# Performance work log

Hardware: AMD Instinct MI355X
Metric: run time of the kernel (lower is better)

## Reference

```python
import jax, jax.numpy as jnp
import numpy as np

N_NODES = 100000
FEAT_DIM = 3
HID = 128
S1 = 50  # enc1 neighbor samples
S2 = 10  # enc2 neighbor samples


def setup_inputs() -> dict:
    key = jax.random.key(0)
    ks = jax.random.split(key, 12)
    inp = {
        "nodes": jnp.arange(N_NODES, dtype=jnp.int64) if jax.config.jax_enable_x64 else jnp.arange(N_NODES, dtype=jnp.int32),
        "features": jax.random.normal(ks[0], (N_NODES, FEAT_DIM), dtype=jnp.float32),
        "neigh1": jax.random.randint(ks[1], (N_NODES, S1), 0, N_NODES),
        "neigh2": jax.random.randint(ks[2], (N_NODES, S2), 0, N_NODES),
        "W1": jax.random.normal(ks[3], (HID, FEAT_DIM), dtype=jnp.float32) * 0.5,
        "W2": jax.random.normal(ks[4], (HID, HID), dtype=jnp.float32) * 0.08,
        "w_a": jax.random.normal(ks[5], (128, HID + 1), dtype=jnp.float32) * 0.08,
        "b_a": jax.random.normal(ks[6], (128,), dtype=jnp.float32) * 0.01,
        "w_b": jax.random.normal(ks[7], (64, 128), dtype=jnp.float32) * 0.08,
        "b_b": jax.random.normal(ks[8], (64,), dtype=jnp.float32) * 0.01,
        "w_c": jax.random.normal(ks[9], (1, 64), dtype=jnp.float32) * 0.1,
        "b_c": jax.random.normal(ks[10], (1,), dtype=jnp.float32) * 0.01,
        "partition_size": 500,
        "n_partition_edges": 137,
    }
    return inp


def reference(nodes, features, neigh1, neigh2, W1, W2, w_a, b_a, w_b, b_b, w_c, b_c,
              partition_size, n_partition_edges):
    # ---- enc1 (GraphSAGE mean, gcn=True: self node included in mean) over all nodes
    nf1 = features[neigh1]                       # [N, S1, F] irregular gather
    agg1 = (nf1.sum(axis=1) + features) / (neigh1.shape[1] + 1)  # [N, F]
    h1 = jax.nn.relu(agg1 @ W1.T)                # [N, HID]

    # ---- enc2 over the query nodes
    nf2 = h1[neigh2[nodes]]                      # [n, S2, HID] irregular gather
    agg2 = (nf2.sum(axis=1) + h1[nodes]) / (neigh2.shape[1] + 1)  # [n, HID]
    emb = jax.nn.relu(agg2 @ W2.T)               # [n, HID]

    # ---- append remaining-space column, MLP, softmax over all nodes (dim 0)
    remaining_space = jnp.asarray(partition_size - n_partition_edges, dtype=emb.dtype)
    col = jnp.full((emb.shape[0], 1), remaining_space, dtype=emb.dtype)
    x = jnp.concatenate([emb, col], axis=1)      # [n, HID+1]
    x = jax.nn.relu(x @ w_a.T + b_a)
    x = jax.nn.relu(x @ w_b.T + b_b)
    scores = (x @ w_c.T + b_c)[:, 0]             # [n]
    return jax.nn.softmax(scores, axis=0)
```

## Files before the change

### kernel.cpp

```cpp
#include <hip/hip_runtime.h>
#include <math.h>

#define N_NODES 100000
#define S1 50
#define S2 10
#define HID 128
#define NT 64
#define AST 66

#define W2_ELEMS   (128 * 128)
#define WA_ELEMS   (129 * 128)
#define WB_ELEMS   (128 * 64)
#define PAD_ELEMS  (W2_ELEMS + WA_ELEMS + WB_ELEMS)

__device__ __forceinline__ unsigned long long dkey(double d) {
    unsigned long long u = __double_as_longlong(d);
    return (u & 0x8000000000000000ULL) ? ~u : (u | 0x8000000000000000ULL);
}
__device__ __forceinline__ double dunkey(unsigned long long k) {
    return (k & 0x8000000000000000ULL)
        ? __longlong_as_double(k & 0x7FFFFFFFFFFFFFFFULL)
        : __longlong_as_double(~k);
}

__global__ __launch_bounds__(256) void pack_kernel(
    const float* __restrict__ feat,
    const float* __restrict__ W2, const float* __restrict__ w_a,
    const float* __restrict__ w_b,
    double* __restrict__ wt, float4* __restrict__ feat4,
    unsigned long long* __restrict__ gmaxu, double* __restrict__ gsum)
{
    int i = blockIdx.x * 256 + threadIdx.x;
    if (i == 0) { gmaxu[0] = 0ULL; gsum[0] = 0.0; }
    if (i < W2_ELEMS) {
        int k = i >> 7, o = i & 127;
        wt[i] = (double)W2[o * 128 + k];
    } else if (i < W2_ELEMS + WA_ELEMS) {
        int j = i - W2_ELEMS;
        int k = j >> 7, o = j & 127;
        wt[i] = (double)w_a[o * 129 + k];
    } else if (i < PAD_ELEMS) {
        int j = i - W2_ELEMS - WA_ELEMS;
        int k = j >> 6, o = j & 63;
        wt[i] = (double)w_b[o * 128 + k];
    } else if (i < PAD_ELEMS + N_NODES) {
        int n = i - PAD_ELEMS;
        float4 v = { feat[n * 3 + 0], feat[n * 3 + 1], feat[n * 3 + 2], 0.0f };
        feat4[n] = v;
    }
}

__global__ __launch_bounds__(64) void gather_kernel(
    const float4* __restrict__ feat4, const int* __restrict__ neigh1,
    double* __restrict__ agg1d)
{
    const int n = blockIdx.x * 64 + threadIdx.x;
    if (n >= N_NODES) return;
    const int* __restrict__ row = &neigh1[n * S1];
    double f0, f1, f2;
    { float4 v = feat4[n]; f0 = (double)v.x; f1 = (double)v.y; f2 = (double)v.z; }
    #pragma unroll 10
    for (int j = 0; j < S1; j++) {
        float4 v = feat4[row[j]];
        f0 += (double)v.x; f1 += (double)v.y; f2 += (double)v.z;
    }
    const double r51 = 1.0 / 51.0;
    agg1d[n * 3 + 0] = f0 * r51;
    agg1d[n * 3 + 1] = f1 * r51;
    agg1d[n * 3 + 2] = f2 * r51;
}

__global__ __launch_bounds__(256, 1) void enc2_mlp_kernel(
    const int* __restrict__ nodes, const int* __restrict__ neigh2,
    const double* __restrict__ agg1d,
    const float* __restrict__ W1, const double* __restrict__ wt,
    const float* __restrict__ b_a, const float* __restrict__ b_b,
    const float* __restrict__ w_c, const float* __restrict__ b_c,
    const int* __restrict__ psz, const int* __restrict__ npe,
    double* __restrict__ scoresd, unsigned long long* __restrict__ gmaxu)
{
    __shared__ __align__(16) double sX[HID * AST];
    __shared__ double sS[4];
    double* sG = sX;

    const double* __restrict__ Wt2 = wt;
    const double* __restrict__ Wta = wt + W2_ELEMS;
    const double* __restrict__ Wtb = wt + W2_ELEMS + WA_ELEMS;

    const int tid  = threadIdx.x;
    const int base = blockIdx.x * NT;

    for (int t = tid; t < NT * (S2 + 1); t += 256) {
        int ns = t / 11, j = t - ns * 11;
        int gi = base + ns;
        int node = nodes[gi < N_NODES ? gi : N_NODES - 1];
        int src  = (j == 0) ? node : neigh2[node * S2 + (j - 1)];
        sG[t * 4 + 0] = agg1d[src * 3 + 0];
        sG[t * 4 + 1] = agg1d[src * 3 + 1];
        sG[t * 4 + 2] = agg1d[src * 3 + 2];
    }
    __syncthreads();

    {
        const int n = tid & 63;
        double g0[11], g1[11], g2[11];
        #pragma unroll
        for (int j = 0; j < 11; j++) {
            g0[j] = sG[(n * 11 + j) * 4 + 0];
            g1[j] = sG[(n * 11 + j) * 4 + 1];
            g2[j] = sG[(n * 11 + j) * 4 + 2];
        }
        __syncthreads();
        const int part = tid >> 6;
        #pragma unroll
        for (int s = 0; s < 32; s++) {
            int t = part * 32 + s;
            double wx = (double)W1[t * 3 + 0];
            double wy = (double)W1[t * 3 + 1];
            double wz = (double)W1[t * 3 + 2];
            double acc = 0.0;
            #pragma unroll
            for (int j = 0; j < 11; j++)
                acc += fmax(wx * g0[j] + wy * g1[j] + wz * g2[j], 0.0);
            sX[t * AST + n] = acc / 11.0;
        }
    }
    __syncthreads();

    const int og = tid & 31;
    const int ng = tid >> 5;
    const int n0 = 8 * ng;
    const int o0 = 2 * og;

    {
        double acc[4][8] = {};
        const double* __restrict__ wk = &Wt2[o0];
        const double* __restrict__ ak = &sX[n0];
        double2 wc0 = *(const double2*)&wk[0];
        double2 wc1 = *(const double2*)&wk[64];
        double2 wd0 = *(const double2*)&wk[128];
        double2 wd1 = *(const double2*)&wk[128 + 64];
        double2 ac[4];
        #pragma unroll
        for (int i = 0; i < 4; i++) ac[i] = *(const double2*)&ak[2 * i];
        #pragma unroll 4
        for (int k = 0; k < 128; k++) {
            const int k1 = (k + 1) & 127;
            const int k2 = (k + 2) & 127;
            double2 wn0 = *(const double2*)&wk[k2 * 128];
            double2 wn1 = *(const double2*)&wk[k2 * 128 + 64];
            double2 an[4];
            #pragma unroll
            for (int i = 0; i < 4; i++)
                an[i] = *(const double2*)&ak[k1 * AST + 2 * i];
            #pragma unroll
            for (int i = 0; i < 4; i++) {
                acc[0][2*i]   += wc0.x * ac[i].x; acc[0][2*i+1] += wc0.x * ac[i].y;
                acc[1][2*i]   += wc0.y * ac[i].x; acc[1][2*i+1] += wc0.y * ac[i].y;
                acc[2][2*i]   += wc1.x * ac[i].x; acc[2][2*i+1] += wc1.x * ac[i].y;
                acc[3][2*i]   += wc1.y * ac[i].x; acc[3][2*i+1] += wc1.y * ac[i].y;
            }
            wc0 = wd0; wc1 = wd1; wd0 = wn0; wd1 = wn1;
            #pragma unroll
            for (int i = 0; i < 4; i++) ac[i] = an[i];
        }
        __syncthreads();
        #pragma unroll
        for (int i = 0; i < 4; i++) {
            int o = (i < 2) ? (o0 + i) : (64 + o0 + i - 2);
            #pragma unroll
            for (int j = 0; j < 4; j++) {
                double2 v = { fmax(acc[i][2*j], 0.0), fmax(acc[i][2*j+1], 0.0) };
                *(double2*)&sX[o * AST + n0 + 2 * j] = v;
            }
        }
    }
    __syncthreads();

    {
        double acc[4][8] = {};
        const double* __restrict__ wk = &Wta[o0];
        const double* __restrict__ ak = &sX[n0];
        double2 wc0 = *(const double2*)&wk[0];
        double2 wc1 = *(const double2*)&wk[64];
        double2 wd0 = *(const double2*)&wk[128];
        double2 wd1 = *(const double2*)&wk[128 + 64];
        double2 ac[4];
        #pragma unroll
        for (int i = 0; i < 4; i++) ac[i] = *(const double2*)&ak[2 * i];
        #pragma unroll 4
        for (int k = 0; k < 128; k++) {
            const int k1 = (k + 1) & 127;
            const int k2 = (k + 2) & 127;
            double2 wn0 = *(const double2*)&wk[k2 * 128];
            double2 wn1 = *(const double2*)&wk[k2 * 128 + 64];
            double2 an[4];
            #pragma unroll
            for (int i = 0; i < 4; i++)
                an[i] = *(const double2*)&ak[k1 * AST + 2 * i];
            #pragma unroll
            for (int i = 0; i < 4; i++) {
                acc[0][2*i]   += wc0.x * ac[i].x; acc[0][2*i+1] += wc0.x * ac[i].y;
                acc[1][2*i]   += wc0.y * ac[i].x; acc[1][2*i+1] += wc0.y * ac[i].y;
                acc[2][2*i]   += wc1.x * ac[i].x; acc[2][2*i+1] += wc1.x * ac[i].y;
                acc[3][2*i]   += wc1.y * ac[i].x; acc[3][2*i+1] += wc1.y * ac[i].y;
            }
            wc0 = wd0; wc1 = wd1; wd0 = wn0; wd1 = wn1;
            #pragma unroll
            for (int i = 0; i < 4; i++) ac[i] = an[i];
        }
        const double rem = (double)(psz[0] - npe[0]);
        double2 rl = *(const double2*)&Wta[128 * 128 + o0];
        double2 rh = *(const double2*)&Wta[128 * 128 + 64 + o0];
        const double ad[4] = {
            rl.x * rem + (double)b_a[o0],
            rl.y * rem + (double)b_a[o0 + 1],
            rh.x * rem + (double)b_a[64 + o0],
            rh.y * rem + (double)b_a[64 + o0 + 1] };
        __syncthreads();
        #pragma unroll
        for (int i = 0; i < 4; i++) {
            int o = (i < 2) ? (o0 + i) : (64 + o0 + i - 2);
            #pragma unroll
            for (int j = 0; j < 4; j++) {
                double2 v = { fmax(acc[i][2*j] + ad[i], 0.0),
                              fmax(acc[i][2*j+1] + ad[i], 0.0) };
                *(double2*)&sX[o * AST + n0 + 2 * j] = v;
            }
        }
    }
    __syncthreads();

    {
        double acc[2][8] = {};
        const double* __restrict__ wk = &Wtb[o0];
        const double* __restrict__ ak = &sX[n0];
        double2 wc = *(const double2*)&wk[0];
        double2 wd = *(const double2*)&wk[64];
        double2 ac[4];
        #pragma unroll
        for (int i = 0; i < 4; i++) ac[i] = *(const double2*)&ak[2 * i];
        #pragma unroll 4
        for (int k = 0; k < 128; k++) {
            const int k1 = (k + 1) & 127;
            const int k2 = (k + 2) & 127;
            double2 wn = *(const double2*)&wk[k2 * 64];
            double2 an[4];
            #pragma unroll
            for (int i = 0; i < 4; i++)
                an[i] = *(const double2*)&ak[k1 * AST + 2 * i];
            #pragma unroll
            for (int i = 0; i < 4; i++) {
                acc[0][2*i]   += wc.x * ac[i].x; acc[0][2*i+1] += wc.x * ac[i].y;
                acc[1][2*i]   += wc.y * ac[i].x; acc[1][2*i+1] += wc.y * ac[i].y;
            }
            wc = wd; wd = wn;
            #pragma unroll
            for (int i = 0; i < 4; i++) ac[i] = an[i];
        }
        __syncthreads();
        #pragma unroll
        for (int i = 0; i < 2; i++) {
            int o = o0 + i;
            double bb = (double)b_b[o];
            #pragma unroll
            for (int j = 0; j < 4; j++) {
                double2 v = { fmax(acc[i][2*j] + bb, 0.0),
                              fmax(acc[i][2*j+1] + bb, 0.0) };
                *(double2*)&sX[o * AST + n0 + 2 * j] = v;
            }
        }
    }
    __syncthreads();

    {
        const int j4 = tid & 3, ns = tid >> 2;
        double v = 0.0;
        #pragma unroll
        for (int r = 0; r < 16; r++)
            v += (double)w_c[j4 + 4 * r] * sX[(j4 + 4 * r) * AST + ns];
        v += __shfl_down(v, 2);
        v += __shfl_down(v, 1);
        double sc = v + (double)b_c[0];
        const bool valid = (base + ns) < N_NODES;
        if (j4 == 0 && valid)
            scoresd[base + ns] = sc;
        double vh = (j4 == 0 && valid) ? sc : -HUGE_VAL;
        #pragma unroll
        for (int off = 32; off > 0; off >>= 1)
            vh = fmax(vh, __shfl_down(vh, off));
        if ((tid & 63) == 0) sS[tid >> 6] = vh;
        __syncthreads();
        if (tid == 0)
            atomicMax(gmaxu, dkey(fmax(fmax(sS[0], sS[1]),
                                       fmax(sS[2], sS[3]))));
    }
}

__global__ __launch_bounds__(256) void exp_sum_kernel(
    double* __restrict__ s, const unsigned long long* __restrict__ gmaxu,
    double* __restrict__ gsum)
{
    __shared__ double red[4];
    const int tid = threadIdx.x;
    const double m = dunkey(gmaxu[0]);

    double acc = 0.0;
    for (int i = blockIdx.x * 256 + tid; i < N_NODES; i += gridDim.x * 256) {
        double e = exp(s[i] - m);
        s[i] = e;
        acc += e;
    }
    #pragma unroll
    for (int off = 32; off > 0; off >>= 1) acc += __shfl_down(acc, off);
    if ((tid & 63) == 0) red[tid >> 6] = acc;
    __syncthreads();
    if (tid == 0)
        atomicAdd(gsum, (red[0] + red[1]) + (red[2] + red[3]));
}

__global__ __launch_bounds__(256) void scale_kernel(
    const double* __restrict__ e, const double* __restrict__ gsum,
    float* __restrict__ out)
{
    __shared__ double sv;
    const int tid = threadIdx.x;
    if (tid == 0) sv = 1.0 / gsum[0];
    __syncthreads();
    const int i = blockIdx.x * 256 + tid;
    if (i < N_NODES) out[i] = (float)(e[i] * sv);
}

extern "C" void kernel_launch(void* const* d_in, const int* in_sizes, int n_in,
                              void* d_out, int out_size, void* d_ws, size_t ws_size,
                              hipStream_t stream)
{
    const int*   nodes = (const int*)  d_in[0];
    const float* feat  = (const float*)d_in[1];
    const int*   n1    = (const int*)  d_in[2];
    const int*   n2    = (const int*)  d_in[3];
    const float* W1    = (const float*)d_in[4];
    const float* W2    = (const float*)d_in[5];
    const float* w_a   = (const float*)d_in[6];
    const float* b_a   = (const float*)d_in[7];
    const float* w_b   = (const float*)d_in[8];
    const float* b_b   = (const float*)d_in[9];
    const float* w_c   = (const float*)d_in[10];
    const float* b_c   = (const float*)d_in[11];
    const int*   psz   = (const int*)  d_in[12];
    const int*   npe   = (const int*)  d_in[13];
    float* out = (float*)d_out;

    double* agg1d   = (double*)d_ws;
    double* scoresd = agg1d + (size_t)N_NODES * 3;
    unsigned long long* gmaxu =
        (unsigned long long*)(scoresd + N_NODES);
    double* gsum    = (double*)(gmaxu + 1);
    double* wt      = scoresd + N_NODES + 16;
    float4* feat4   = (float4*)(wt + PAD_ELEMS);

    const int pack_blocks = (PAD_ELEMS + N_NODES + 255) / 256;
    pack_kernel<<<pack_blocks, 256, 0, stream>>>(
        feat, W2, w_a, w_b, wt, feat4, gmaxu, gsum);
    gather_kernel<<<(N_NODES + 63) / 64, 64, 0, stream>>>(feat4, n1, agg1d);
    enc2_mlp_kernel<<<(N_NODES + NT - 1) / NT, 256, 0, stream>>>(
        nodes, n2, agg1d, W1, wt, b_a, b_b, w_c, b_c, psz, npe, scoresd, gmaxu);
    exp_sum_kernel<<<256, 256, 0, stream>>>(scoresd, gmaxu, gsum);
    scale_kernel<<<(N_NODES + 255) / 256, 256, 0, stream>>>(scoresd, gsum, out);
}
```

Measured before the change: 356.3 us.

## Fuse softmax exp-sum and scale into one kernel with grid barrier; pair neighbor loads

Merges the exp/sum kernel and the scale kernel into one launch of 196 blocks. Each thread keeps its two exponentials in registers, and the blocks wait on an atomic counter acting as a grid-wide barrier before normalizing. This removes one launch and the write and re-read of the exp values. The neighbor gather in the first stage now loads index pairs as int2 and issues two feature loads per iteration. The spin barrier only works if all 196 blocks are resident at once, which should hold on this device.

```diff
diff --git a/kernel.cpp b/kernel.cpp
--- a/kernel.cpp
+++ b/kernel.cpp
@@ -7,6 +7,7 @@
 #define HID 128
 #define NT 64
 #define AST 66
+#define SM_BLOCKS 196
 
 #define W2_ELEMS   (128 * 128)
 #define WA_ELEMS   (129 * 128)
@@ -28,10 +29,11 @@
     const float* __restrict__ W2, const float* __restrict__ w_a,
     const float* __restrict__ w_b,
     double* __restrict__ wt, float4* __restrict__ feat4,
-    unsigned long long* __restrict__ gmaxu, double* __restrict__ gsum)
+    unsigned long long* __restrict__ gmaxu, double* __restrict__ gsum,
+    int* __restrict__ done)
 {
     int i = blockIdx.x * 256 + threadIdx.x;
-    if (i == 0) { gmaxu[0] = 0ULL; gsum[0] = 0.0; }
+    if (i == 0) { gmaxu[0] = 0ULL; gsum[0] = 0.0; done[0] = 0; }
     if (i < W2_ELEMS) {
         int k = i >> 7, o = i & 127;
         wt[i] = (double)W2[o * 128 + k];
@@ -56,13 +58,17 @@
 {
     const int n = blockIdx.x * 64 + threadIdx.x;
     if (n >= N_NODES) return;
-    const int* __restrict__ row = &neigh1[n * S1];
+    const int2* __restrict__ row2 = (const int2*)&neigh1[n * S1];
     double f0, f1, f2;
     { float4 v = feat4[n]; f0 = (double)v.x; f1 = (double)v.y; f2 = (double)v.z; }
-    #pragma unroll 10
-    for (int j = 0; j < S1; j++) {
-        float4 v = feat4[row[j]];
-        f0 += (double)v.x; f1 += (double)v.y; f2 += (double)v.z;
+    #pragma unroll 5
+    for (int j = 0; j < S1 / 2; j++) {
+        int2 p = row2[j];
+        float4 a = feat4[p.x];
+        float4 b = feat4[p.y];
+        f0 += (double)a.x + (double)b.x;
+        f1 += (double)a.y + (double)b.y;
+        f2 += (double)a.z + (double)b.z;
     }
     const double r51 = 1.0 / 51.0;
     agg1d[n * 3 + 0] = f0 * r51;
@@ -297,38 +303,42 @@
     }
 }
 
-__global__ __launch_bounds__(256) void exp_sum_kernel(
-    double* __restrict__ s, const unsigned long long* __restrict__ gmaxu,
-    double* __restrict__ gsum)
+__global__ __launch_bounds__(256) void softmax_kernel(
+    const double* __restrict__ s, const unsigned long long* __restrict__ gmaxu,
+    double* __restrict__ gsum, int* __restrict__ done,
+    float* __restrict__ out)
 {
     __shared__ double red[4];
+    __shared__ double sinv;
     const int tid = threadIdx.x;
     const double m = dunkey(gmaxu[0]);
-
-    double acc = 0.0;
-    for (int i = blockIdx.x * 256 + tid; i < N_NODES; i += gridDim.x * 256) {
-        double e = exp(s[i] - m);
-        s[i] = e;
-        acc += e;
-    }
+    const int i0 = blockIdx.x * 256 + tid;
+    const int i1 = i0 + SM_BLOCKS * 256;
+
+    double e0 = 0.0, e1 = 0.0, acc = 0.0;
+    if (i0 < N_NODES) { e0 = exp(s[i0] - m); acc += e0; }
+    if (i1 < N_NODES) { e1 = exp(s[i1] - m); acc += e1; }
+
     #pragma unroll
     for (int off = 32; off > 0; off >>= 1) acc += __shfl_down(acc, off);
     if ((tid & 63) == 0) red[tid >> 6] = acc;
     __syncthreads();
-    if (tid == 0)
+    if (tid == 0) {
         atomicAdd(gsum, (red[0] + red[1]) + (red[2] + red[3]));
-}
-
-__global__ __launch_bounds__(256) void scale_kernel(
-    const double* __restrict__ e, const double* __restrict__ gsum,
-    float* __restrict__ out)
-{
-    __shared__ double sv;
-    const int tid = threadIdx.x;
-    if (tid == 0) sv = 1.0 / gsum[0];
-    __syncthreads();
-    const int i = blockIdx.x * 256 + tid;
-    if (i < N_NODES) out[i] = (float)(e[i] * sv);
+        __threadfence();
+        atomicAdd(done, 1);
+        while (__hip_atomic_load(done, __ATOMIC_RELAXED,
+                                 __HIP_MEMORY_SCOPE_AGENT) < SM_BLOCKS) {
+            __builtin_amdgcn_s_sleep(1);
+        }
+        __threadfence();
+        sinv = 1.0 / __hip_atomic_load(gsum, __ATOMIC_RELAXED,
+                                       __HIP_MEMORY_SCOPE_AGENT);
+    }
+    __syncthreads();
+    const double invS = sinv;
+    if (i0 < N_NODES) out[i0] = (float)(e0 * invS);
+    if (i1 < N_NODES) out[i1] = (float)(e1 * invS);
 }
 
 extern "C" void kernel_launch(void* const* d_in, const int* in_sizes, int n_in,
@@ -356,15 +366,15 @@
     unsigned long long* gmaxu =
         (unsigned long long*)(scoresd + N_NODES);
     double* gsum    = (double*)(gmaxu + 1);
+    int*    done    = (int*)(gsum + 1);
     double* wt      = scoresd + N_NODES + 16;
     float4* feat4   = (float4*)(wt + PAD_ELEMS);
 
     const int pack_blocks = (PAD_ELEMS + N_NODES + 255) / 256;
     pack_kernel<<<pack_blocks, 256, 0, stream>>>(
-        feat, W2, w_a, w_b, wt, feat4, gmaxu, gsum);
+        feat, W2, w_a, w_b, wt, feat4, gmaxu, gsum, done);
     gather_kernel<<<(N_NODES + 63) / 64, 64, 0, stream>>>(feat4, n1, agg1d);
     enc2_mlp_kernel<<<(N_NODES + NT - 1) / NT, 256, 0, stream>>>(
         nodes, n2, agg1d, W1, wt, b_a, b_b, w_c, b_c, psz, npe, scoresd, gmaxu);
-    exp_sum_kernel<<<256, 256, 0, stream>>>(scoresd, gmaxu, gsum);
-    scale_kernel<<<(N_NODES + 255) / 256, 256, 0, stream>>>(scoresd, gsum, out);
-}
+    softmax_kernel<<<SM_BLOCKS, 256, 0, stream>>>(scoresd, gmaxu, gsum, done, out);
+}
```

Measured after the change: 367.9 us. +3.2%, slower.
